# Optimization experiments

Measured on AMD Instinct MI355X. Metric: run time of the kernel, lower is better.

## Reference

```python
import jax, jax.numpy as jnp
import numpy as np

DIM = 3072
KV_DIM = 2048
HEADS = 16
DIM_HEAD = 128
INNER = HEADS * DIM_HEAD  # 2048
EPS = 1e-5


def layer_norm(x, g, b):
    mu = jnp.mean(x, axis=-1, keepdims=True)
    var = jnp.var(x, axis=-1, keepdims=True)
    return (x - mu) * jax.lax.rsqrt(var + EPS) * g + b


def setup_inputs() -> dict:
    key = jax.random.key(0)
    ks = jax.random.split(key, 8)
    b, n1, n2 = 2, 2048, 2048
    x = jax.random.normal(ks[0], (b, n1, KV_DIM), dtype=jnp.float32)
    latents = jax.random.normal(ks[1], (b, n2, DIM), dtype=jnp.float32)
    w_q = jax.random.normal(ks[2], (DIM, INNER), dtype=jnp.float32) / np.sqrt(DIM)
    w_kv = jax.random.normal(ks[3], (KV_DIM, 2 * INNER), dtype=jnp.float32) / np.sqrt(KV_DIM)
    w_out = jax.random.normal(ks[4], (INNER, DIM), dtype=jnp.float32) / np.sqrt(INNER)
    ln1_g = jnp.ones((KV_DIM,), jnp.float32)
    ln1_b = jnp.zeros((KV_DIM,), jnp.float32)
    ln2_g = jnp.ones((DIM,), jnp.float32)
    ln2_b = jnp.zeros((DIM,), jnp.float32)
    return {"x": x, "latents": latents, "w_q": w_q, "w_kv": w_kv,
            "w_out": w_out, "ln1_g": ln1_g, "ln1_b": ln1_b,
            "ln2_g": ln2_g, "ln2_b": ln2_b}


def reference(x, latents, w_q, w_kv, w_out, ln1_g, ln1_b, ln2_g, ln2_b):
    b, n2, _ = latents.shape
    xn = layer_norm(x, ln1_g, ln1_b)            # (b, n1, kv_dim)
    ln = layer_norm(latents, ln2_g, ln2_b)      # (b, n2, dim)
    q = ln @ w_q                                # (b, n2, inner)
    kv = xn @ w_kv                              # (b, n1, 2*inner)
    k, v = jnp.split(kv, 2, axis=-1)
    # (b, h, n, d)
    def split_heads(t):
        bs, n, _ = t.shape
        return t.reshape(bs, n, HEADS, DIM_HEAD).transpose(0, 2, 1, 3)
    q, k, v = split_heads(q), split_heads(k), split_heads(v)
    scale = 1.0 / np.sqrt(np.sqrt(DIM_HEAD)).astype(np.float32)
    w = jnp.einsum('bhqd,bhkd->bhqk', q * scale, k * scale)
    w = jax.nn.softmax(w.astype(jnp.float32), axis=-1).astype(q.dtype)
    out = jnp.einsum('bhqk,bhkd->bhqd', w, v)
    out = out.transpose(0, 2, 1, 3).reshape(b, n2, INNER)
    return out @ w_out
```

## Files before the change

kernel.cpp:

```cpp
#include <hip/hip_runtime.h>
#include <type_traits>


using u16 = unsigned short;
using u32 = unsigned int;
typedef __attribute__((ext_vector_type(8))) short short8;
typedef __attribute__((ext_vector_type(4))) float floatx4;

typedef __attribute__((address_space(1))) const unsigned int gu32;
typedef __attribute__((address_space(3))) unsigned int lu32;

__device__ __forceinline__ void gld16(void* lds, const void* g) {
  __builtin_amdgcn_global_load_lds((gu32*)g, (lu32*)lds, 16, 0, 0);
}

__device__ inline u16 f2bf(float f) {
  u32 u = __float_as_uint(f);
  u32 r = (u + 0x7FFFu + ((u >> 16) & 1u)) >> 16;
  return (u16)r;
}

template <int L>
__global__ __launch_bounds__(256) void ln_cast(const float* __restrict__ in,
                                               const float* __restrict__ gw,
                                               const float* __restrict__ bw,
                                               u16* __restrict__ out) {
  constexpr int C4 = L / 1024;
  const int row = blockIdx.x;
  const int t = threadIdx.x;
  const float* rp = in + (size_t)row * L;
  float4 v[C4];
  float s = 0.f, ss = 0.f;
#pragma unroll
  for (int c = 0; c < C4; ++c) {
    v[c] = *(const float4*)(rp + (c * 256 + t) * 4);
    s += v[c].x + v[c].y + v[c].z + v[c].w;
    ss += v[c].x * v[c].x + v[c].y * v[c].y + v[c].z * v[c].z + v[c].w * v[c].w;
  }
#pragma unroll
  for (int off = 32; off > 0; off >>= 1) {
    s += __shfl_down(s, off);
    ss += __shfl_down(ss, off);
  }
  __shared__ float red[8];
  const int wave = t >> 6, lane = t & 63;
  if (lane == 0) { red[wave] = s; red[4 + wave] = ss; }
  __syncthreads();
  const float tot = red[0] + red[1] + red[2] + red[3];
  const float tss = red[4] + red[5] + red[6] + red[7];
  const float mu = tot * (1.f / L);
  const float rstd = rsqrtf(tss * (1.f / L) - mu * mu + 1e-5f);
  u16* op = out + (size_t)row * L;
#pragma unroll
  for (int c = 0; c < C4; ++c) {
    const int base = (c * 256 + t) * 4;
    float4 gv = *(const float4*)(gw + base);
    float4 bv = *(const float4*)(bw + base);
    u32 p0 = (u32)f2bf((v[c].x - mu) * rstd * gv.x + bv.x) |
             ((u32)f2bf((v[c].y - mu) * rstd * gv.y + bv.y) << 16);
    u32 p1 = (u32)f2bf((v[c].z - mu) * rstd * gv.z + bv.z) |
             ((u32)f2bf((v[c].w - mu) * rstd * gv.w + bv.w) << 16);
    uint2 pk; pk.x = p0; pk.y = p1;
    *(uint2*)(op + base) = pk;
  }
}

__global__ __launch_bounds__(256) void transpose_cast(const float* __restrict__ in,
                                                      u16* __restrict__ out,
                                                      int R, int C) {
  __shared__ u16 tile[32][33];
  const int c0 = blockIdx.x * 32, r0 = blockIdx.y * 32;
  const int x = threadIdx.x, y = threadIdx.y;
#pragma unroll
  for (int j = 0; j < 4; ++j)
    tile[y + 8 * j][x] = f2bf(in[(size_t)(r0 + y + 8 * j) * C + c0 + x]);
  __syncthreads();
#pragma unroll
  for (int j = 0; j < 4; ++j)
    out[(size_t)(c0 + y + 8 * j) * R + r0 + x] = tile[x][y + 8 * j];
}

__global__ __launch_bounds__(256) void transpose_v(const u16* __restrict__ kvb,
                                                   u16* __restrict__ vT) {
  __shared__ u16 tile[32][33];
  const int bh = blockIdx.z, b = bh >> 4, h = bh & 15;
  const u16* src = kvb + (size_t)b * 2048 * 4096 + 2048 + h * 128;
  u16* dst = vT + (size_t)bh * 128 * 2048;
  const int d0 = blockIdx.x * 32, n0 = blockIdx.y * 32;
  const int x = threadIdx.x, y = threadIdx.y;
#pragma unroll
  for (int j = 0; j < 4; ++j)
    tile[y + 8 * j][x] = src[(size_t)(n0 + y + 8 * j) * 4096 + d0 + x];
  __syncthreads();
#pragma unroll
  for (int j = 0; j < 4; ++j)
    dst[(size_t)(d0 + y + 8 * j) * 2048 + n0 + x] = tile[x][y + 8 * j];
}

template <typename OutT>
__global__ __launch_bounds__(256) void gemm_bt(const u16* __restrict__ A,
                                               const u16* __restrict__ Bt,
                                               OutT* __restrict__ C,
                                               int M, int N, int K) {
  __shared__ u16 As[128 * 64];
  __shared__ u16 Bs[128 * 64];
  const int tid = threadIdx.x;
  const int wave = tid >> 6, lane = tid & 63, l16 = lane & 15, quad = lane >> 4;
  const int wm = (wave >> 1) * 64, wn = (wave & 1) * 64;
  const long m0 = (long)blockIdx.y * 128, n0 = (long)blockIdx.x * 128;
  const int srow = tid >> 3;
  const int gc = ((tid & 7) ^ ((tid >> 3) & 7)) * 8;
  const u16* Ag0 = A + (m0 + srow) * (long)K + gc;
  const u16* Bg0 = Bt + (n0 + srow) * (long)K + gc;
  const long rowoff = 32L * K;

  const floatx4 fz = {0.f, 0.f, 0.f, 0.f};
  floatx4 acc[4][4];
#pragma unroll
  for (int i = 0; i < 4; ++i)
#pragma unroll
    for (int j = 0; j < 4; ++j) acc[i][j] = fz;

  for (int k0 = 0; k0 < K; k0 += 64) {
    __syncthreads();
#pragma unroll
    for (int c = 0; c < 4; ++c) {
      gld16(&As[(c * 256 + tid) * 8], Ag0 + c * rowoff + k0);
      gld16(&Bs[(c * 256 + tid) * 8], Bg0 + c * rowoff + k0);
    }
    __syncthreads();
#pragma unroll
    for (int kd = 0; kd < 2; ++kd) {
      const int sw = ((4 * kd + quad) ^ (l16 & 7)) * 8;
      short8 a[4], b[4];
#pragma unroll
      for (int i = 0; i < 4; ++i) a[i] = *(const short8*)&As[(wm + i * 16 + l16) * 64 + sw];
#pragma unroll
      for (int j = 0; j < 4; ++j) b[j] = *(const short8*)&Bs[(wn + j * 16 + l16) * 64 + sw];
#pragma unroll
      for (int i = 0; i < 4; ++i)
#pragma unroll
        for (int j = 0; j < 4; ++j)
          acc[i][j] = __builtin_amdgcn_mfma_f32_16x16x32_bf16(a[i], b[j], acc[i][j], 0, 0, 0);
    }
  }

#pragma unroll
  for (int i = 0; i < 4; ++i)
#pragma unroll
    for (int r = 0; r < 4; ++r) {
      const long row = m0 + wm + i * 16 + quad * 4 + r;
#pragma unroll
      for (int j = 0; j < 4; ++j) {
        const long col = n0 + wn + j * 16 + l16;
        if constexpr (std::is_same<OutT, float>::value)
          C[row * N + col] = acc[i][j][r];
        else
          C[row * N + col] = f2bf(acc[i][j][r]);
      }
    }
}

#define GBAR()                                         \
  do {                                                 \
    asm volatile("" ::: "memory");                     \
    __builtin_amdgcn_s_barrier();                      \
    asm volatile("" ::: "memory");                     \
  } while (0)
#define VMW(N) asm volatile("s_waitcnt vmcnt(" #N ")" ::: "memory")

#define G8_LDA(MH)                                                             \
  {                                                                            \
    const u16* Ab_ = &As[buf][(MH) * 8192 + (wr * 32 + l16) * 64];             \
    _Pragma("unroll") for (int mi = 0; mi < 2; ++mi)                           \
    _Pragma("unroll") for (int ks = 0; ks < 2; ++ks)                           \
      af[mi][ks] = *(const short8*)&Ab_[mi * 1024 + ((4 * ks + quad) ^ swz) * 8]; \
  }
#define G8_LDB(DST, NH)                                                        \
  {                                                                            \
    const u16* Bb_ = &Bs[buf][(NH) * 8192 + (wc * 64 + l16) * 64];             \
    _Pragma("unroll") for (int ni = 0; ni < 4; ++ni)                           \
    _Pragma("unroll") for (int ks = 0; ks < 2; ++ks)                           \
      DST[ni][ks] = *(const short8*)&Bb_[ni * 1024 + ((4 * ks + quad) ^ swz) * 8]; \
  }
#define G8_MFMA(MH, BFX, NH)                                                   \
  __builtin_amdgcn_s_setprio(1);                                               \
  _Pragma("unroll") for (int ks = 0; ks < 2; ++ks)                             \
  _Pragma("unroll") for (int mi = 0; mi < 2; ++mi)                             \
  _Pragma("unroll") for (int ni = 0; ni < 4; ++ni)                             \
    acc[MH][mi][NH][ni] = __builtin_amdgcn_mfma_f32_16x16x32_bf16(             \
        af[mi][ks], BFX[ni][ks], acc[MH][mi][NH][ni], 0, 0, 0);                \
  __builtin_amdgcn_s_setprio(0);

template <typename OutT>
__global__ __launch_bounds__(512, 2) void gemm_bt8(const u16* __restrict__ A,
                                                   const u16* __restrict__ Bt,
                                                   OutT* __restrict__ C,
                                                   int M, int N, int K) {
  __shared__ u16 As[2][16384];
  __shared__ u16 Bs[2][16384];
  (void)M;
  const int tid = threadIdx.x;
  const int wave = tid >> 6, lane = tid & 63, l16 = lane & 15, quad = lane >> 4;
  const int wr = wave >> 1;
  const int wc = wave & 1;
  const int nwg = gridDim.x * gridDim.y;
  const int bid0 = blockIdx.y * gridDim.x + blockIdx.x;
  const int bid = (bid0 & 7) * (nwg >> 3) + (bid0 >> 3);
  const int bx = bid % gridDim.x, by = bid / gridDim.x;
  const long m0 = (long)by * 256, n0 = (long)bx * 256;

  const int srow = tid >> 3;
  const int gc = ((tid & 7) ^ (srow & 7)) * 8;

  auto stageA = [&](int bufn, int h, int k0) {
#pragma unroll
    for (int c = 0; c < 2; ++c)
      gld16(&As[bufn][h * 8192 + (c * 512 + tid) * 8],
            A + (size_t)(m0 + h * 128 + c * 64 + srow) * K + k0 + gc);
  };
  auto stageB = [&](int bufn, int h, int k0) {
#pragma unroll
    for (int c = 0; c < 2; ++c)
      gld16(&Bs[bufn][h * 8192 + (c * 512 + tid) * 8],
            Bt + (size_t)(n0 + h * 128 + c * 64 + srow) * K + k0 + gc);
  };

  const floatx4 fz = {0.f, 0.f, 0.f, 0.f};
  floatx4 acc[2][2][2][4];
#pragma unroll
  for (int a = 0; a < 2; ++a)
#pragma unroll
    for (int b = 0; b < 2; ++b)
#pragma unroll
      for (int c = 0; c < 2; ++c)
#pragma unroll
        for (int d = 0; d < 4; ++d) acc[a][b][c][d] = fz;

  short8 af[2][2], bf0[4][2], bf1[4][2];
  const int swz = l16 & 7;

  stageA(0, 0, 0);
  stageB(0, 0, 0);
  stageB(0, 1, 0);
  stageA(0, 1, 0);
  VMW(4);
  GBAR();

  const int NT = K >> 6;
  for (int t = 0; t < NT; ++t) {
    const int buf = t & 1;
    const int kn = (t + 1) << 6;
    const bool pre = (t + 1 < NT);

    G8_LDA(0);
    G8_LDB(bf0, 0);
    if (pre) stageA(buf ^ 1, 0, kn);
    GBAR();
    G8_MFMA(0, bf0, 0);
    if (pre) { VMW(4); } else { VMW(2); }
    GBAR();

    G8_LDB(bf1, 1);
    if (pre) stageB(buf ^ 1, 0, kn);
    GBAR();
    G8_MFMA(0, bf1, 1);
    if (pre) { VMW(4); } else { VMW(0); }
    GBAR();

    G8_LDA(1);
    if (pre) stageB(buf ^ 1, 1, kn);
    GBAR();
    G8_MFMA(1, bf0, 0);
    GBAR();

    if (pre) stageA(buf ^ 1, 1, kn);
    GBAR();
    G8_MFMA(1, bf1, 1);
    if (pre) { VMW(4); }
    GBAR();
  }

#pragma unroll
  for (int mh = 0; mh < 2; ++mh)
#pragma unroll
    for (int mi = 0; mi < 2; ++mi)
#pragma unroll
      for (int rr = 0; rr < 4; ++rr) {
        const long row = m0 + mh * 128 + wr * 32 + mi * 16 + quad * 4 + rr;
#pragma unroll
        for (int nh = 0; nh < 2; ++nh)
#pragma unroll
          for (int ni = 0; ni < 4; ++ni) {
            const long col = n0 + nh * 128 + wc * 64 + ni * 16 + l16;
            if constexpr (std::is_same<OutT, float>::value)
              C[row * N + col] = acc[mh][mi][nh][ni][rr];
            else
              C[row * N + col] = f2bf(acc[mh][mi][nh][ni][rr]);
          }
      }
}

#undef G8_LDA
#undef G8_LDB
#undef G8_MFMA

__global__ __launch_bounds__(256, 2) void flash_attn(const u16* __restrict__ Q,
                                                     const u16* __restrict__ KV,
                                                     const u16* __restrict__ VT,
                                                     u16* __restrict__ O) {
  __shared__ u16 Ks[2][64 * 128];
  __shared__ u16 Vs[2][128 * 64];
  __shared__ u16 Ps[4][32 * 64];
  const int tid = threadIdx.x;
  const int wave = tid >> 6, lane = tid & 63, l16 = lane & 15, quad = lane >> 4;
  const int d = blockIdx.x;
  const int bh = (d & 7) * 4 + ((d >> 3) & 3);
  const int qt = d >> 5;
  const int b = bh >> 4, h = bh & 15;
  const u16* Qb = Q + (size_t)b * 2048 * 2048 + h * 128;
  const u16* Kb = KV + (size_t)b * 2048 * 4096 + h * 128;
  const u16* Vb = VT + (size_t)bh * 128 * 2048;
  u16* Ob = O + (size_t)b * 2048 * 2048 + h * 128;
  const int q0 = qt * 128 + wave * 32;

  short8 qf[2][4];
#pragma unroll
  for (int t = 0; t < 2; ++t)
#pragma unroll
    for (int kd = 0; kd < 4; ++kd)
      qf[t][kd] = *(const short8*)&Qb[(size_t)(q0 + t * 16 + l16) * 2048 + kd * 32 + quad * 8];

  short8 onesf;
  {
    union { short8 s; u32 w[4]; } uo;
    const u32 o = (l16 == 0) ? 0x3F803F80u : 0u;
#pragma unroll
    for (int i = 0; i < 4; ++i) uo.w[i] = o;
    onesf = uo.s;
  }

  const floatx4 fz = {0.f, 0.f, 0.f, 0.f};
  floatx4 oacc[2][9];
  float m[2][4];
#pragma unroll
  for (int t = 0; t < 2; ++t) {
#pragma unroll
    for (int jd = 0; jd < 9; ++jd) oacc[t][jd] = fz;
#pragma unroll
    for (int r = 0; r < 4; ++r) m[t][r] = -1e30f;
  }

  u16* Psw = Ps[wave];
  const float sc2 = 0.12751775f;
  const float THR2 = 11.5416f;

  auto stage = [&](int buf, int kv0) {
#pragma unroll
    for (int c = 0; c < 4; ++c) {
      const int li = c * 256 + tid;
      const int krow = li >> 4, kdb = (li & 15) ^ (krow & 15);
      gld16(&Ks[buf][li * 8], Kb + (size_t)(kv0 + krow) * 4096 + kdb * 8);
      const int vrow = li >> 3, vdb = (li & 7) ^ (vrow & 7);
      gld16(&Vs[buf][li * 8], Vb + (size_t)vrow * 2048 + kv0 + vdb * 8);
    }
  };

  stage(0, 0);
  int cur = 0;

  for (int kt = 0; kt < 32; ++kt) {
    __syncthreads();
    if (kt < 31) stage(cur ^ 1, (kt + 1) * 64);
    const u16* Kc = Ks[cur];
    const u16* Vc = Vs[cur];

    floatx4 sacc[2][4];
#pragma unroll
    for (int t = 0; t < 2; ++t)
#pragma unroll
      for (int jn = 0; jn < 4; ++jn) sacc[t][jn] = fz;
    __builtin_amdgcn_s_setprio(1);
#pragma unroll
    for (int jn = 0; jn < 4; ++jn)
#pragma unroll
      for (int kd = 0; kd < 4; ++kd) {
        short8 kb = *(const short8*)&Kc[(jn * 16 + l16) * 128 + ((4 * kd + quad) ^ l16) * 8];
        sacc[0][jn] = __builtin_amdgcn_mfma_f32_16x16x32_bf16(qf[0][kd], kb, sacc[0][jn], 0, 0, 0);
        sacc[1][jn] = __builtin_amdgcn_mfma_f32_16x16x32_bf16(qf[1][kd], kb, sacc[1][jn], 0, 0, 0);
      }
    __builtin_amdgcn_s_setprio(0);

#pragma unroll
    for (int t = 0; t < 2; ++t) {
#pragma unroll
      for (int r = 0; r < 4; ++r) {
        float mx = fmaxf(fmaxf(sacc[t][0][r], sacc[t][1][r]),
                         fmaxf(sacc[t][2][r], sacc[t][3][r]));
#pragma unroll
        for (int off = 8; off > 0; off >>= 1) mx = fmaxf(mx, __shfl_xor(mx, off, 16));
        const float mxs = sc2 * mx;
        if (!__all(mxs - m[t][r] <= THR2)) {
          const float mnew = fmaxf(m[t][r], mxs);
          const float alpha = __builtin_amdgcn_exp2f(m[t][r] - mnew);
          m[t][r] = mnew;
#pragma unroll
          for (int jd = 0; jd < 9; ++jd) oacc[t][jd][r] *= alpha;
        }
        const float mrow = m[t][r];
        const int q = t * 16 + quad * 4 + r;
        const int mask = (q & 7) ^ (q >> 3);
        u16* prow = &Psw[q * 64 + (l16 & 7)];
#pragma unroll
        for (int jn = 0; jn < 4; ++jn) {
          const float p = __builtin_amdgcn_exp2f(fmaf(sc2, sacc[t][jn][r], -mrow));
          const int slot = (2 * jn + (l16 >> 3)) ^ mask;
          prow[slot * 8] = f2bf(p);
        }
      }
    }

    const int pmask0 = (l16 & 7) ^ (l16 >> 3);
    const int pmask1 = (l16 & 7) ^ (2 + (l16 >> 3));
    __builtin_amdgcn_s_setprio(1);
#pragma unroll
    for (int kk = 0; kk < 2; ++kk) {
      const int chunk = 4 * kk + quad;
      short8 pf0 = *(const short8*)&Psw[(l16) * 64 + (chunk ^ pmask0) * 8];
      short8 pf1 = *(const short8*)&Psw[(16 + l16) * 64 + (chunk ^ pmask1) * 8];
#pragma unroll
      for (int jd = 0; jd < 8; ++jd) {
        short8 vb = *(const short8*)&Vc[(jd * 16 + l16) * 64 + (chunk ^ (l16 & 7)) * 8];
        oacc[0][jd] = __builtin_amdgcn_mfma_f32_16x16x32_bf16(pf0, vb, oacc[0][jd], 0, 0, 0);
        oacc[1][jd] = __builtin_amdgcn_mfma_f32_16x16x32_bf16(pf1, vb, oacc[1][jd], 0, 0, 0);
      }
      oacc[0][8] = __builtin_amdgcn_mfma_f32_16x16x32_bf16(pf0, onesf, oacc[0][8], 0, 0, 0);
      oacc[1][8] = __builtin_amdgcn_mfma_f32_16x16x32_bf16(pf1, onesf, oacc[1][8], 0, 0, 0);
    }
    __builtin_amdgcn_s_setprio(0);
    cur ^= 1;
  }

#pragma unroll
  for (int t = 0; t < 2; ++t)
#pragma unroll
    for (int r = 0; r < 4; ++r) {
      const float l = __shfl(oacc[t][8][r], lane & 48);
      const float inv = 1.f / l;
      const size_t row = q0 + t * 16 + quad * 4 + r;
#pragma unroll
      for (int jd = 0; jd < 8; ++jd)
        Ob[row * 2048 + jd * 16 + l16] = f2bf(oacc[t][jd][r] * inv);
    }
}

extern "C" void kernel_launch(void* const* d_in, const int* in_sizes, int n_in,
                              void* d_out, int out_size, void* d_ws, size_t ws_size,
                              hipStream_t stream) {
  const float* x       = (const float*)d_in[0];
  const float* latents = (const float*)d_in[1];
  const float* w_q     = (const float*)d_in[2];
  const float* w_kv    = (const float*)d_in[3];
  const float* w_out   = (const float*)d_in[4];
  const float* ln1_g   = (const float*)d_in[5];
  const float* ln1_b   = (const float*)d_in[6];
  const float* ln2_g   = (const float*)d_in[7];
  const float* ln2_b   = (const float*)d_in[8];

  char* ws = (char*)d_ws;
  u16* xn    = (u16*)(ws);
  u16* lnl   = (u16*)(ws + 16777216);
  u16* wqT   = (u16*)(ws + 41943040);
  u16* wkvT  = (u16*)(ws + 54525952);
  u16* woutT = (u16*)(ws + 71303168);
  u16* qb    = (u16*)(ws + 83886080);
  u16* kvb   = (u16*)(ws + 100663296);
  u16* vTb   = lnl;
  u16* attn  = xn;

  ln_cast<2048><<<dim3(4096), 256, 0, stream>>>(x, ln1_g, ln1_b, xn);
  ln_cast<3072><<<dim3(4096), 256, 0, stream>>>(latents, ln2_g, ln2_b, lnl);

  transpose_cast<<<dim3(64, 96), dim3(32, 8), 0, stream>>>(w_q, wqT, 3072, 2048);
  transpose_cast<<<dim3(128, 64), dim3(32, 8), 0, stream>>>(w_kv, wkvT, 2048, 4096);
  transpose_cast<<<dim3(96, 64), dim3(32, 8), 0, stream>>>(w_out, woutT, 2048, 3072);

  gemm_bt<u16><<<dim3(16, 32), 256, 0, stream>>>(lnl, wqT, qb, 4096, 2048, 3072);
  gemm_bt8<u16><<<dim3(16, 16), 512, 0, stream>>>(xn, wkvT, kvb, 4096, 4096, 2048);

  transpose_v<<<dim3(4, 64, 32), dim3(32, 8), 0, stream>>>(kvb, vTb);

  flash_attn<<<dim3(512), 256, 0, stream>>>(qb, kvb, vTb, attn);

  gemm_bt8<float><<<dim3(12, 16), 512, 0, stream>>>(attn, woutT, (float*)d_out, 4096, 3072, 2048);
}
```

Before: 513.3 us.

## Fuse V transpose into KV GEMM epilogue and software-pipeline PV in flash attention

The KV projection GEMM now writes the V half directly in transposed per-head layout from its epilogue, which removes the separate transpose_v kernel and its extra read/write pass. The flash attention loop is restructured so the P·V MFMAs for the previous tile run right after the current QK^T MFMAs, with K and V staged separately around an added barrier. The aim is to overlap softmax and V loads with matrix work. The cost is an extra __syncthreads per iteration and scattered 8-byte stores in the GEMM epilogue.

After: 525.2 us. +2.3%, slower.

```diff
diff --git a/kernel.cpp b/kernel.cpp
--- a/kernel.cpp
+++ b/kernel.cpp
@@ -6,6 +6,7 @@
 using u32 = unsigned int;
 typedef __attribute__((ext_vector_type(8))) short short8;
 typedef __attribute__((ext_vector_type(4))) float floatx4;
+typedef __attribute__((ext_vector_type(4))) unsigned short u16x4;
 
 typedef __attribute__((address_space(1))) const unsigned int gu32;
 typedef __attribute__((address_space(3))) unsigned int lu32;
@@ -78,23 +79,6 @@
 #pragma unroll
   for (int j = 0; j < 4; ++j)
     out[(size_t)(c0 + y + 8 * j) * R + r0 + x] = tile[x][y + 8 * j];
-}
-
-__global__ __launch_bounds__(256) void transpose_v(const u16* __restrict__ kvb,
-                                                   u16* __restrict__ vT) {
-  __shared__ u16 tile[32][33];
-  const int bh = blockIdx.z, b = bh >> 4, h = bh & 15;
-  const u16* src = kvb + (size_t)b * 2048 * 4096 + 2048 + h * 128;
-  u16* dst = vT + (size_t)bh * 128 * 2048;
-  const int d0 = blockIdx.x * 32, n0 = blockIdx.y * 32;
-  const int x = threadIdx.x, y = threadIdx.y;
-#pragma unroll
-  for (int j = 0; j < 4; ++j)
-    tile[y + 8 * j][x] = src[(size_t)(n0 + y + 8 * j) * 4096 + d0 + x];
-  __syncthreads();
-#pragma unroll
-  for (int j = 0; j < 4; ++j)
-    dst[(size_t)(d0 + y + 8 * j) * 2048 + n0 + x] = tile[x][y + 8 * j];
 }
 
 template <typename OutT>
@@ -196,7 +180,9 @@
 __global__ __launch_bounds__(512, 2) void gemm_bt8(const u16* __restrict__ A,
                                                    const u16* __restrict__ Bt,
                                                    OutT* __restrict__ C,
-                                                   int M, int N, int K) {
+                                                   int M, int N, int K,
+                                                   u16* __restrict__ vT,
+                                                   int vcol0) {
   __shared__ u16 As[2][16384];
   __shared__ u16 Bs[2][16384];
   (void)M;
@@ -281,24 +267,47 @@
     GBAR();
   }
 
-#pragma unroll
-  for (int mh = 0; mh < 2; ++mh)
-#pragma unroll
-    for (int mi = 0; mi < 2; ++mi)
-#pragma unroll
-      for (int rr = 0; rr < 4; ++rr) {
-        const long row = m0 + mh * 128 + wr * 32 + mi * 16 + quad * 4 + rr;
+  bool vpath = false;
+  if constexpr (std::is_same<OutT, u16>::value) vpath = (n0 >= vcol0);
+  if (vpath) {
+#pragma unroll
+    for (int mh = 0; mh < 2; ++mh)
+#pragma unroll
+      for (int mi = 0; mi < 2; ++mi) {
+        const long row_base = m0 + mh * 128 + wr * 32 + mi * 16 + quad * 4;
+        const long bb = row_base >> 11, nn = row_base & 2047;
 #pragma unroll
         for (int nh = 0; nh < 2; ++nh)
 #pragma unroll
           for (int ni = 0; ni < 4; ++ni) {
-            const long col = n0 + nh * 128 + wc * 64 + ni * 16 + l16;
-            if constexpr (std::is_same<OutT, float>::value)
-              C[row * N + col] = acc[mh][mi][nh][ni][rr];
-            else
-              C[row * N + col] = f2bf(acc[mh][mi][nh][ni][rr]);
+            const long col = n0 + nh * 128 + wc * 64 + ni * 16 + l16 - vcol0;
+            const long hh = col >> 7, dd = col & 127;
+            u16x4 pk;
+#pragma unroll
+            for (int rr = 0; rr < 4; ++rr) pk[rr] = f2bf(acc[mh][mi][nh][ni][rr]);
+            *(u16x4*)&vT[(((bb * 16 + hh) * 128 + dd) << 11) + nn] = pk;
           }
       }
+  } else {
+#pragma unroll
+    for (int mh = 0; mh < 2; ++mh)
+#pragma unroll
+      for (int mi = 0; mi < 2; ++mi)
+#pragma unroll
+        for (int rr = 0; rr < 4; ++rr) {
+          const long row = m0 + mh * 128 + wr * 32 + mi * 16 + quad * 4 + rr;
+#pragma unroll
+          for (int nh = 0; nh < 2; ++nh)
+#pragma unroll
+            for (int ni = 0; ni < 4; ++ni) {
+              const long col = n0 + nh * 128 + wc * 64 + ni * 16 + l16;
+              if constexpr (std::is_same<OutT, float>::value)
+                C[row * N + col] = acc[mh][mi][nh][ni][rr];
+              else
+                C[row * N + col] = f2bf(acc[mh][mi][nh][ni][rr]);
+            }
+        }
+  }
 }
 
 #undef G8_LDA
@@ -354,26 +363,35 @@
   u16* Psw = Ps[wave];
   const float sc2 = 0.12751775f;
   const float THR2 = 11.5416f;
-
-  auto stage = [&](int buf, int kv0) {
+  const int pmask0 = (l16 & 7) ^ (l16 >> 3);
+  const int pmask1 = (l16 & 7) ^ (2 + (l16 >> 3));
+
+  auto stageK = [&](int buf, int kv0) {
 #pragma unroll
     for (int c = 0; c < 4; ++c) {
       const int li = c * 256 + tid;
       const int krow = li >> 4, kdb = (li & 15) ^ (krow & 15);
       gld16(&Ks[buf][li * 8], Kb + (size_t)(kv0 + krow) * 4096 + kdb * 8);
+    }
+  };
+  auto stageV = [&](int buf, int kv0) {
+#pragma unroll
+    for (int c = 0; c < 4; ++c) {
+      const int li = c * 256 + tid;
       const int vrow = li >> 3, vdb = (li & 7) ^ (vrow & 7);
       gld16(&Vs[buf][li * 8], Vb + (size_t)vrow * 2048 + kv0 + vdb * 8);
     }
   };
 
-  stage(0, 0);
+  stageK(0, 0);
+  stageV(0, 0);
   int cur = 0;
 
   for (int kt = 0; kt < 32; ++kt) {
     __syncthreads();
-    if (kt < 31) stage(cur ^ 1, (kt + 1) * 64);
+    if (kt < 31) stageK(cur ^ 1, (kt + 1) * 64);
     const u16* Kc = Ks[cur];
-    const u16* Vc = Vs[cur];
+    const u16* Vp = Vs[cur ^ 1];
 
     floatx4 sacc[2][4];
 #pragma unroll
@@ -389,7 +407,26 @@
         sacc[0][jn] = __builtin_amdgcn_mfma_f32_16x16x32_bf16(qf[0][kd], kb, sacc[0][jn], 0, 0, 0);
         sacc[1][jn] = __builtin_amdgcn_mfma_f32_16x16x32_bf16(qf[1][kd], kb, sacc[1][jn], 0, 0, 0);
       }
+    if (kt > 0) {
+#pragma unroll
+      for (int kk = 0; kk < 2; ++kk) {
+        const int chunk = 4 * kk + quad;
+        short8 pf0 = *(const short8*)&Psw[(l16) * 64 + (chunk ^ pmask0) * 8];
+        short8 pf1 = *(const short8*)&Psw[(16 + l16) * 64 + (chunk ^ pmask1) * 8];
+#pragma unroll
+        for (int jd = 0; jd < 8; ++jd) {
+          short8 vb = *(const short8*)&Vp[(jd * 16 + l16) * 64 + (chunk ^ (l16 & 7)) * 8];
+          oacc[0][jd] = __builtin_amdgcn_mfma_f32_16x16x32_bf16(pf0, vb, oacc[0][jd], 0, 0, 0);
+          oacc[1][jd] = __builtin_amdgcn_mfma_f32_16x16x32_bf16(pf1, vb, oacc[1][jd], 0, 0, 0);
+        }
+        oacc[0][8] = __builtin_amdgcn_mfma_f32_16x16x32_bf16(pf0, onesf, oacc[0][8], 0, 0, 0);
+        oacc[1][8] = __builtin_amdgcn_mfma_f32_16x16x32_bf16(pf1, onesf, oacc[1][8], 0, 0, 0);
+      }
+    }
     __builtin_amdgcn_s_setprio(0);
+
+    __syncthreads();
+    if (kt < 31) stageV(cur ^ 1, (kt + 1) * 64);
 
 #pragma unroll
     for (int t = 0; t < 2; ++t) {
@@ -419,9 +456,11 @@
         }
       }
     }
-
-    const int pmask0 = (l16 & 7) ^ (l16 >> 3);
-    const int pmask1 = (l16 & 7) ^ (2 + (l16 >> 3));
+    cur ^= 1;
+  }
+
+  {
+    const u16* Vp = Vs[cur ^ 1];
     __builtin_amdgcn_s_setprio(1);
 #pragma unroll
     for (int kk = 0; kk < 2; ++kk) {
@@ -430,7 +469,7 @@
       short8 pf1 = *(const short8*)&Psw[(16 + l16) * 64 + (chunk ^ pmask1) * 8];
 #pragma unroll
       for (int jd = 0; jd < 8; ++jd) {
-        short8 vb = *(const short8*)&Vc[(jd * 16 + l16) * 64 + (chunk ^ (l16 & 7)) * 8];
+        short8 vb = *(const short8*)&Vp[(jd * 16 + l16) * 64 + (chunk ^ (l16 & 7)) * 8];
         oacc[0][jd] = __builtin_amdgcn_mfma_f32_16x16x32_bf16(pf0, vb, oacc[0][jd], 0, 0, 0);
         oacc[1][jd] = __builtin_amdgcn_mfma_f32_16x16x32_bf16(pf1, vb, oacc[1][jd], 0, 0, 0);
       }
@@ -438,7 +477,6 @@
       oacc[1][8] = __builtin_amdgcn_mfma_f32_16x16x32_bf16(pf1, onesf, oacc[1][8], 0, 0, 0);
     }
     __builtin_amdgcn_s_setprio(0);
-    cur ^= 1;
   }
 
 #pragma unroll
@@ -486,11 +524,12 @@
   transpose_cast<<<dim3(96, 64), dim3(32, 8), 0, stream>>>(w_out, woutT, 2048, 3072);
 
   gemm_bt<u16><<<dim3(16, 32), 256, 0, stream>>>(lnl, wqT, qb, 4096, 2048, 3072);
-  gemm_bt8<u16><<<dim3(16, 16), 512, 0, stream>>>(xn, wkvT, kvb, 4096, 4096, 2048);
-
-  transpose_v<<<dim3(4, 64, 32), dim3(32, 8), 0, stream>>>(kvb, vTb);
+  gemm_bt8<u16><<<dim3(16, 16), 512, 0, stream>>>(xn, wkvT, kvb, 4096, 4096, 2048,
+                                                  vTb, 2048);
 
   flash_attn<<<dim3(512), 256, 0, stream>>>(qb, kvb, vTb, attn);
 
-  gemm_bt8<float><<<dim3(12, 16), 512, 0, stream>>>(attn, woutT, (float*)d_out, 4096, 3072, 2048);
-}
+  gemm_bt8<float><<<dim3(12, 16), 512, 0, stream>>>(attn, woutT, (float*)d_out,
+                                                    4096, 3072, 2048, nullptr,
+                                                    1 << 30);
+}
```

## Fuse V transpose into KV projection GEMM epilogue via LDS staging

Applied to the files above, without the earlier changes.

Removes the separate transpose_v kernel. Output tiles of the KV GEMM that fall in the V half are staged transposed through LDS and written straight into the per-head V^T buffer with vectorized 16-byte stores. This saves a kernel launch and a full read and write of V. In exchange the V half of the KV buffer is no longer written, and the epilogue gains extra barriers and LDS traffic.

New measurement: 506.0 us. Within noise of the previous version (-1.4%).

```diff
diff --git a/kernel.cpp b/kernel.cpp
--- a/kernel.cpp
+++ b/kernel.cpp
@@ -6,6 +6,7 @@
 using u32 = unsigned int;
 typedef __attribute__((ext_vector_type(8))) short short8;
 typedef __attribute__((ext_vector_type(4))) float floatx4;
+typedef __attribute__((ext_vector_type(4))) unsigned short u16x4;
 
 typedef __attribute__((address_space(1))) const unsigned int gu32;
 typedef __attribute__((address_space(3))) unsigned int lu32;
@@ -78,23 +79,6 @@
 #pragma unroll
   for (int j = 0; j < 4; ++j)
     out[(size_t)(c0 + y + 8 * j) * R + r0 + x] = tile[x][y + 8 * j];
-}
-
-__global__ __launch_bounds__(256) void transpose_v(const u16* __restrict__ kvb,
-                                                   u16* __restrict__ vT) {
-  __shared__ u16 tile[32][33];
-  const int bh = blockIdx.z, b = bh >> 4, h = bh & 15;
-  const u16* src = kvb + (size_t)b * 2048 * 4096 + 2048 + h * 128;
-  u16* dst = vT + (size_t)bh * 128 * 2048;
-  const int d0 = blockIdx.x * 32, n0 = blockIdx.y * 32;
-  const int x = threadIdx.x, y = threadIdx.y;
-#pragma unroll
-  for (int j = 0; j < 4; ++j)
-    tile[y + 8 * j][x] = src[(size_t)(n0 + y + 8 * j) * 4096 + d0 + x];
-  __syncthreads();
-#pragma unroll
-  for (int j = 0; j < 4; ++j)
-    dst[(size_t)(d0 + y + 8 * j) * 2048 + n0 + x] = tile[x][y + 8 * j];
 }
 
 template <typename OutT>
@@ -196,7 +180,9 @@
 __global__ __launch_bounds__(512, 2) void gemm_bt8(const u16* __restrict__ A,
                                                    const u16* __restrict__ Bt,
                                                    OutT* __restrict__ C,
-                                                   int M, int N, int K) {
+                                                   int M, int N, int K,
+                                                   u16* __restrict__ vT,
+                                                   int vcol0) {
   __shared__ u16 As[2][16384];
   __shared__ u16 Bs[2][16384];
   (void)M;
@@ -281,24 +267,57 @@
     GBAR();
   }
 
-#pragma unroll
-  for (int mh = 0; mh < 2; ++mh)
-#pragma unroll
-    for (int mi = 0; mi < 2; ++mi)
-#pragma unroll
-      for (int rr = 0; rr < 4; ++rr) {
-        const long row = m0 + mh * 128 + wr * 32 + mi * 16 + quad * 4 + rr;
-#pragma unroll
-        for (int nh = 0; nh < 2; ++nh)
+  bool vpath = false;
+  if constexpr (std::is_same<OutT, u16>::value) vpath = (n0 >= vcol0);
+  if (vpath) {
+    u16* tl = (u16*)&As[0][0];
+#pragma unroll
+    for (int mh = 0; mh < 2; ++mh)
+#pragma unroll
+      for (int nh = 0; nh < 2; ++nh) {
+        const long R0 = m0 + mh * 128;
+        const long bb = R0 >> 11, nn0 = R0 & 2047;
+        const long hh = (n0 + nh * 128 - vcol0) >> 7;
+        __syncthreads();
+        const int dl0 = wc * 64 + l16;
+        const int nl0 = wr * 32 + quad * 4;
+#pragma unroll
+        for (int mi = 0; mi < 2; ++mi)
 #pragma unroll
           for (int ni = 0; ni < 4; ++ni) {
-            const long col = n0 + nh * 128 + wc * 64 + ni * 16 + l16;
-            if constexpr (std::is_same<OutT, float>::value)
-              C[row * N + col] = acc[mh][mi][nh][ni][rr];
-            else
-              C[row * N + col] = f2bf(acc[mh][mi][nh][ni][rr]);
+            u16x4 pk;
+#pragma unroll
+            for (int rr = 0; rr < 4; ++rr) pk[rr] = f2bf(acc[mh][mi][nh][ni][rr]);
+            *(u16x4*)&tl[(dl0 + ni * 16) * 136 + nl0 + mi * 16] = pk;
           }
+        __syncthreads();
+        const int d = tid >> 2, sg = (tid & 3) * 32;
+        u16* gp = &vT[(((bb * 16 + hh) * 128 + d) << 11) + nn0 + sg];
+        const u16* lp = &tl[d * 136 + sg];
+#pragma unroll
+        for (int j = 0; j < 4; ++j)
+          *(short8*)&gp[j * 8] = *(const short8*)&lp[j * 8];
       }
+  } else {
+#pragma unroll
+    for (int mh = 0; mh < 2; ++mh)
+#pragma unroll
+      for (int mi = 0; mi < 2; ++mi)
+#pragma unroll
+        for (int rr = 0; rr < 4; ++rr) {
+          const long row = m0 + mh * 128 + wr * 32 + mi * 16 + quad * 4 + rr;
+#pragma unroll
+          for (int nh = 0; nh < 2; ++nh)
+#pragma unroll
+            for (int ni = 0; ni < 4; ++ni) {
+              const long col = n0 + nh * 128 + wc * 64 + ni * 16 + l16;
+              if constexpr (std::is_same<OutT, float>::value)
+                C[row * N + col] = acc[mh][mi][nh][ni][rr];
+              else
+                C[row * N + col] = f2bf(acc[mh][mi][nh][ni][rr]);
+            }
+        }
+  }
 }
 
 #undef G8_LDA
@@ -486,11 +505,12 @@
   transpose_cast<<<dim3(96, 64), dim3(32, 8), 0, stream>>>(w_out, woutT, 2048, 3072);
 
   gemm_bt<u16><<<dim3(16, 32), 256, 0, stream>>>(lnl, wqT, qb, 4096, 2048, 3072);
-  gemm_bt8<u16><<<dim3(16, 16), 512, 0, stream>>>(xn, wkvT, kvb, 4096, 4096, 2048);
-
-  transpose_v<<<dim3(4, 64, 32), dim3(32, 8), 0, stream>>>(kvb, vTb);
+  gemm_bt8<u16><<<dim3(16, 16), 512, 0, stream>>>(xn, wkvT, kvb, 4096, 4096, 2048,
+                                                  vTb, 2048);
 
   flash_attn<<<dim3(512), 256, 0, stream>>>(qb, kvb, vTb, attn);
 
-  gemm_bt8<float><<<dim3(12, 16), 512, 0, stream>>>(attn, woutT, (float*)d_out, 4096, 3072, 2048);
-}
+  gemm_bt8<float><<<dim3(12, 16), 512, 0, stream>>>(attn, woutT, (float*)d_out,
+                                                    4096, 3072, 2048, nullptr,
+                                                    1 << 30);
+}
```
